# Kernel tuning notes

Hardware: AMD Instinct MI355X
Metric: run time of the kernel (lower is better)

## Reference

```python
import jax, jax.numpy as jnp
import numpy as np

EPS = 1e-12  # torch F.normalize eps

def _l2norm(x):
    n = jnp.linalg.norm(x, axis=-1, keepdims=True)
    return x / jnp.maximum(n, EPS)

def setup_inputs() -> dict:
    key = jax.random.key(0)
    k0, k1, k2, k3 = jax.random.split(key, 4)
    B, S, L, E, N = 16, 2048, 512, 512, 2048
    z = jax.random.normal(k0, (B, S, L), dtype=jnp.float32)
    mask = jnp.ones((B, S), dtype=bool)  # unused by the module's forward body
    # learned params (xavier-ish scales)
    W_in = jax.random.normal(k1, (E, L), dtype=jnp.float32) / np.float32(np.sqrt(L))
    b_in = jnp.zeros((E,), dtype=jnp.float32)
    W_out = jax.random.normal(k2, (L, E), dtype=jnp.float32) / np.float32(np.sqrt(E))
    b_out = jnp.zeros((L,), dtype=jnp.float32)
    emb = jax.random.normal(k3, (N, E), dtype=jnp.float32) / np.float32(np.sqrt(E))
    return {"z": z, "mask": mask, "W_in": W_in, "b_in": b_in, "W_out": W_out, "b_out": b_out, "emb": emb}

def reference(z, mask, W_in, b_in, W_out, b_out, emb):
    B, S, L = z.shape
    zf = z.reshape(B * S, L)
    zf = zf @ W_in.T + b_in                 # (BS, E) input projection
    zf = _l2norm(zf)                        # F.normalize over dim=1
    emb_n = _l2norm(emb)                    # codebook rows normalized in-place in torch
    d = -(zf @ emb_n.T)                     # (BS, N) negative cosine similarity
    min_encoding_indices = jnp.argmin(d, axis=1)   # (BS,)
    zq = emb_n[min_encoding_indices]        # gather codebook vectors (BS, E)
    zq = zq @ W_out.T + b_out               # output projection (BS, L)
    zq = zq.reshape(B, S, L)
    zq = z + jax.lax.stop_gradient(zq - z)  # straight-through estimator
    return zq, min_encoding_indices
```

## Files before the change

### kernel.cpp

```cpp
#include <hip/hip_runtime.h>
#include <math.h>

#define BS_TOK 32768
#define DIM 512
#define NCODE 2048

typedef _Float16 f16x8 __attribute__((ext_vector_type(8)));
typedef _Float16 f16x4 __attribute__((ext_vector_type(4)));
typedef float f32x16 __attribute__((ext_vector_type(16)));

#define LDH 40

#define LGKM0_FENCE asm volatile("s_waitcnt lgkmcnt(0)" ::: "memory")
#define SBAR __builtin_amdgcn_s_barrier()

__global__ __launch_bounds__(256) void k_rownorm_split(
    const float* __restrict__ in, _Float16* __restrict__ hi,
    _Float16* __restrict__ lo, int rstride) {
  const int r = blockIdx.x;
  const int t = threadIdx.x;
  const float* row = in + (size_t)r * DIM;
  float v0 = row[t];
  float v1 = row[t + 256];
  float s = v0 * v0 + v1 * v1;
#pragma unroll
  for (int off = 32; off > 0; off >>= 1) s += __shfl_down(s, off, 64);
  __shared__ float ls[4];
  if ((t & 63) == 0) ls[t >> 6] = s;
  __syncthreads();
  float tot = ls[0] + ls[1] + ls[2] + ls[3];
  float sc = 1.0f / fmaxf(sqrtf(tot), 1e-12f);
  float x0 = v0 * sc, x1 = v1 * sc;
  _Float16 h0 = (_Float16)x0;
  _Float16 h1 = (_Float16)x1;
  _Float16 e0 = (_Float16)((x0 - (float)h0) * 2048.0f);
  _Float16 e1 = (_Float16)((x1 - (float)h1) * 2048.0f);
  _Float16* hrow = hi + (size_t)r * rstride;
  _Float16* lrow = lo + (size_t)r * rstride;
  hrow[t] = h0;
  hrow[t + 256] = h1;
  lrow[t] = e0;
  lrow[t + 256] = e1;
}

__global__ __launch_bounds__(256) void k_split_w(const float* __restrict__ w,
                                                 _Float16* __restrict__ hi,
                                                 _Float16* __restrict__ lo) {
  int t = (blockIdx.x * 256 + threadIdx.x) * 4;
  float4 v = *(const float4*)(w + t);
  f16x4 h, l;
  h.x = (_Float16)v.x; l.x = (_Float16)((v.x - (float)h.x) * 2048.0f);
  h.y = (_Float16)v.y; l.y = (_Float16)((v.y - (float)h.y) * 2048.0f);
  h.z = (_Float16)v.z; l.z = (_Float16)((v.z - (float)h.z) * 2048.0f);
  h.w = (_Float16)v.w; l.w = (_Float16)((v.w - (float)h.w) * 2048.0f);
  *(f16x4*)(hi + t) = h;
  *(f16x4*)(lo + t) = l;
}

__global__ __launch_bounds__(256, 2) void k_gemm_mfma_in(
    const float* __restrict__ A, const _Float16* __restrict__ Bhi,
    const _Float16* __restrict__ Blo, const float* __restrict__ bias,
    _Float16* __restrict__ zf16) {
  __shared__ __align__(16) _Float16 sm[2][4][128 * LDH];
  const int tid = threadIdx.x;
  const int w = tid >> 6, l = tid & 63;
  const int wm = w >> 1, wn = w & 1;
  const int lm = l & 31, lh = l >> 5;
  const int m0 = blockIdx.y * 128;
  const int n0 = blockIdx.x * 128;
  const int arow = tid >> 3;
  const int ac4 = (tid & 7) << 2;
  const int brow = tid >> 2;
  const int bq = (tid & 3) << 3;

  f32x16 aHH[2][2], aX[2][2];
#pragma unroll
  for (int mb = 0; mb < 2; ++mb)
#pragma unroll
    for (int nb = 0; nb < 2; ++nb) {
      aHH[mb][nb] = (f32x16)0.0f;
      aX[mb][nb] = (f32x16)0.0f;
    }

  float4 ar[4];
  f16x8 brh[2], brl[2];

  auto LOADS = [&](int kt) {
#pragma unroll
    for (int i = 0; i < 4; ++i)
      ar[i] =
          *(const float4*)(A + (size_t)(m0 + arow + 32 * i) * DIM + kt * 32 + ac4);
#pragma unroll
    for (int i = 0; i < 2; ++i) {
      const size_t g = (size_t)(n0 + brow + 64 * i) * DIM + kt * 32 + bq;
      brh[i] = *(const f16x8*)(Bhi + g);
      brl[i] = *(const f16x8*)(Blo + g);
    }
  };
  auto WRITES = [&](int b) {
#pragma unroll
    for (int i = 0; i < 4; ++i) {
      f16x4 h, lo4;
      h.x = (_Float16)ar[i].x; lo4.x = (_Float16)((ar[i].x - (float)h.x) * 2048.0f);
      h.y = (_Float16)ar[i].y; lo4.y = (_Float16)((ar[i].y - (float)h.y) * 2048.0f);
      h.z = (_Float16)ar[i].z; lo4.z = (_Float16)((ar[i].z - (float)h.z) * 2048.0f);
      h.w = (_Float16)ar[i].w; lo4.w = (_Float16)((ar[i].w - (float)h.w) * 2048.0f);
      *(f16x4*)(&sm[b][0][(arow + 32 * i) * LDH + ac4]) = h;
      *(f16x4*)(&sm[b][1][(arow + 32 * i) * LDH + ac4]) = lo4;
    }
#pragma unroll
    for (int i = 0; i < 2; ++i) {
      *(f16x8*)(&sm[b][2][(brow + 64 * i) * LDH + bq]) = brh[i];
      *(f16x8*)(&sm[b][3][(brow + 64 * i) * LDH + bq]) = brl[i];
    }
  };

  LOADS(0);
  WRITES(0);
  LOADS(1);
  LGKM0_FENCE;
  SBAR;
  int cur = 0;
  const int NT = DIM / 32;
  for (int t = 0; t < NT; ++t) {
    if (t < NT - 1) WRITES(cur ^ 1);
    if (t < NT - 2) LOADS(t + 2);
#pragma unroll
    for (int c = 0; c < 2; ++c) {
      const int ko = c * 16 + lh * 8;
      f16x8 ah[2], al[2], bh[2], bl[2];
#pragma unroll
      for (int mb = 0; mb < 2; ++mb) {
        int r = wm * 64 + mb * 32 + lm;
        ah[mb] = *(const f16x8*)(&sm[cur][0][r * LDH + ko]);
        al[mb] = *(const f16x8*)(&sm[cur][1][r * LDH + ko]);
      }
#pragma unroll
      for (int nb = 0; nb < 2; ++nb) {
        int r = wn * 64 + nb * 32 + lm;
        bh[nb] = *(const f16x8*)(&sm[cur][2][r * LDH + ko]);
        bl[nb] = *(const f16x8*)(&sm[cur][3][r * LDH + ko]);
      }
#pragma unroll
      for (int mb = 0; mb < 2; ++mb)
#pragma unroll
        for (int nb = 0; nb < 2; ++nb) {
          aHH[mb][nb] = __builtin_amdgcn_mfma_f32_32x32x16_f16(
              ah[mb], bh[nb], aHH[mb][nb], 0, 0, 0);
          aX[mb][nb] = __builtin_amdgcn_mfma_f32_32x32x16_f16(
              ah[mb], bl[nb], aX[mb][nb], 0, 0, 0);
          aX[mb][nb] = __builtin_amdgcn_mfma_f32_32x32x16_f16(
              al[mb], bh[nb], aX[mb][nb], 0, 0, 0);
        }
    }
    LGKM0_FENCE;
    SBAR;
    cur ^= 1;
  }
#pragma unroll
  for (int nb = 0; nb < 2; ++nb) {
    int n = n0 + wn * 64 + nb * 32 + lm;
    float bv = bias[n];
#pragma unroll
    for (int mb = 0; mb < 2; ++mb)
#pragma unroll
      for (int r = 0; r < 16; ++r) {
        int m = m0 + wm * 64 + mb * 32 + (r & 3) + 8 * (r >> 2) + 4 * lh;
        float val = aHH[mb][nb][r] + aX[mb][nb][r] * (1.0f / 2048.0f) + bv;
        _Float16 h = (_Float16)val;
        _Float16 lo = (_Float16)((val - (float)h) * 2048.0f);
        zf16[(size_t)m * 1024 + n] = h;
        zf16[(size_t)m * 1024 + 512 + n] = lo;
      }
  }
}

__global__ __launch_bounds__(256, 2) void k_gemm_codebook(
    const _Float16* __restrict__ Ahi, const _Float16* __restrict__ Alo,
    const _Float16* __restrict__ Bhi, const _Float16* __restrict__ Blo,
    const float* __restrict__ bias, float* __restrict__ table) {
  __shared__ __align__(16) _Float16 sm[2][4][128 * LDH];
  const int tid = threadIdx.x;
  const int w = tid >> 6, l = tid & 63;
  const int wm = w >> 1, wn = w & 1;
  const int lm = l & 31, lh = l >> 5;
  const int m0 = blockIdx.y * 128;
  const int n0 = blockIdx.x * 128;
  const int brow = tid >> 2;
  const int bq = (tid & 3) << 3;

  f32x16 aHH[2][2], aX[2][2];
#pragma unroll
  for (int mb = 0; mb < 2; ++mb)
#pragma unroll
    for (int nb = 0; nb < 2; ++nb) {
      aHH[mb][nb] = (f32x16)0.0f;
      aX[mb][nb] = (f32x16)0.0f;
    }

  f16x8 arh[2], arl[2], brh[2], brl[2];

  auto LOADS = [&](int kt) {
    const int kc = kt * 32 + bq;
#pragma unroll
    for (int i = 0; i < 2; ++i) {
      const size_t ga = (size_t)(m0 + brow + 64 * i) * DIM + kc;
      arh[i] = *(const f16x8*)(Ahi + ga);
      arl[i] = *(const f16x8*)(Alo + ga);
      const size_t g = (size_t)(n0 + brow + 64 * i) * DIM + kc;
      brh[i] = *(const f16x8*)(Bhi + g);
      brl[i] = *(const f16x8*)(Blo + g);
    }
  };
  auto WRITES = [&](int b) {
#pragma unroll
    for (int i = 0; i < 2; ++i) {
      *(f16x8*)(&sm[b][0][(brow + 64 * i) * LDH + bq]) = arh[i];
      *(f16x8*)(&sm[b][1][(brow + 64 * i) * LDH + bq]) = arl[i];
      *(f16x8*)(&sm[b][2][(brow + 64 * i) * LDH + bq]) = brh[i];
      *(f16x8*)(&sm[b][3][(brow + 64 * i) * LDH + bq]) = brl[i];
    }
  };

  LOADS(0);
  WRITES(0);
  LOADS(1);
  LGKM0_FENCE;
  SBAR;
  int cur = 0;
  const int NT = DIM / 32;
  for (int t = 0; t < NT; ++t) {
    if (t < NT - 1) WRITES(cur ^ 1);
    if (t < NT - 2) LOADS(t + 2);
#pragma unroll
    for (int c = 0; c < 2; ++c) {
      const int ko = c * 16 + lh * 8;
      f16x8 ah[2], al[2], bh[2], bl[2];
#pragma unroll
      for (int mb = 0; mb < 2; ++mb) {
        int r = wm * 64 + mb * 32 + lm;
        ah[mb] = *(const f16x8*)(&sm[cur][0][r * LDH + ko]);
        al[mb] = *(const f16x8*)(&sm[cur][1][r * LDH + ko]);
      }
#pragma unroll
      for (int nb = 0; nb < 2; ++nb) {
        int r = wn * 64 + nb * 32 + lm;
        bh[nb] = *(const f16x8*)(&sm[cur][2][r * LDH + ko]);
        bl[nb] = *(const f16x8*)(&sm[cur][3][r * LDH + ko]);
      }
#pragma unroll
      for (int mb = 0; mb < 2; ++mb)
#pragma unroll
        for (int nb = 0; nb < 2; ++nb) {
          aHH[mb][nb] = __builtin_amdgcn_mfma_f32_32x32x16_f16(
              ah[mb], bh[nb], aHH[mb][nb], 0, 0, 0);
          aX[mb][nb] = __builtin_amdgcn_mfma_f32_32x32x16_f16(
              ah[mb], bl[nb], aX[mb][nb], 0, 0, 0);
          aX[mb][nb] = __builtin_amdgcn_mfma_f32_32x32x16_f16(
              al[mb], bh[nb], aX[mb][nb], 0, 0, 0);
        }
    }
    LGKM0_FENCE;
    SBAR;
    cur ^= 1;
  }
#pragma unroll
  for (int nb = 0; nb < 2; ++nb) {
    int n = n0 + wn * 64 + nb * 32 + lm;
    float bv = bias[n];
#pragma unroll
    for (int mb = 0; mb < 2; ++mb)
#pragma unroll
      for (int r = 0; r < 16; ++r) {
        int m = m0 + wm * 64 + mb * 32 + (r & 3) + 8 * (r >> 2) + 4 * lh;
        table[(size_t)m * DIM + n] =
            aHH[mb][nb][r] + aX[mb][nb][r] * (1.0f / 2048.0f) + bv;
      }
  }
}

__global__ __launch_bounds__(256) void k_gather_st(
    const float* __restrict__ z, const float* __restrict__ table,
    const int* __restrict__ idx, float* __restrict__ out) {
  int g = blockIdx.x * 256 + threadIdx.x;
  int m = g >> 7;
  int c = (g & 127) << 2;
  int n = idx[m];
  float4 t = *(const float4*)(table + (size_t)n * DIM + c);
  float4 zv = *(const float4*)(z + (size_t)m * DIM + c);
  float4 o;
  o.x = zv.x + (t.x - zv.x);
  o.y = zv.y + (t.y - zv.y);
  o.z = zv.z + (t.z - zv.z);
  o.w = zv.w + (t.w - zv.w);
  *(float4*)(out + (size_t)m * DIM + c) = o;
}

#define SIMK_BM 128
#define SIMK_BN 128
#define NQUART 4
#define QCODES (NCODE / NQUART)

__global__ __launch_bounds__(256, 4) void k_sim_argmax(
    const _Float16* __restrict__ Apack,
    const _Float16* __restrict__ Bhi, unsigned* __restrict__ cand) {
  __shared__ __align__(16) _Float16 sm[2][2][128 * LDH];
  float* sC = (float*)sm;

  const int tid = threadIdx.x;
  const int w = tid >> 6, l = tid & 63;
  const int wm = w >> 1, wn = w & 1;
  const int lm = l & 31, lh = l >> 5;
  const int q = blockIdx.x & (NQUART - 1);
  const int tokbase = (blockIdx.x >> 2) * SIMK_BM;
  const int code0 = q * QCODES;
  const int brow = tid >> 2;
  const int bq = (tid & 3) << 3;
  const int t_red = tid >> 1, h_red = tid & 1;

  unsigned e0 = 0, e1 = 0, e2 = 0, e3 = 0;

  f16x8 arh[2], brh[2];

  auto LOADS = [&](int nt, int kt) {
    const int kc = kt * 32 + bq;
#pragma unroll
    for (int i = 0; i < 2; ++i) {
      arh[i] =
          *(const f16x8*)(Apack + (size_t)(tokbase + brow + 64 * i) * 1024 + kc);
      brh[i] =
          *(const f16x8*)(Bhi + (size_t)(code0 + nt + brow + 64 * i) * DIM + kc);
    }
  };
  auto WRITES = [&](int b) {
#pragma unroll
    for (int i = 0; i < 2; ++i) {
      *(f16x8*)(&sm[b][0][(brow + 64 * i) * LDH + bq]) = arh[i];
      *(f16x8*)(&sm[b][1][(brow + 64 * i) * LDH + bq]) = brh[i];
    }
  };

  for (int nt = 0; nt < QCODES; nt += SIMK_BN) {
    f32x16 aHH[2][2];
#pragma unroll
    for (int mb = 0; mb < 2; ++mb)
#pragma unroll
      for (int nb = 0; nb < 2; ++nb) aHH[mb][nb] = (f32x16)0.0f;
    __syncthreads();
    LOADS(nt, 0);
    WRITES(0);
    LOADS(nt, 1);
    LGKM0_FENCE;
    SBAR;
    int cur = 0;
    for (int t = 0; t < 16; ++t) {
      if (t < 15) WRITES(cur ^ 1);
      if (t < 14) LOADS(nt, t + 2);
#pragma unroll
      for (int c = 0; c < 2; ++c) {
        const int ko = c * 16 + lh * 8;
        f16x8 ah[2], bh[2];
#pragma unroll
        for (int mb = 0; mb < 2; ++mb)
          ah[mb] = *(const f16x8*)(&sm[cur][0][(wm * 64 + mb * 32 + lm) * LDH + ko]);
#pragma unroll
        for (int nb = 0; nb < 2; ++nb)
          bh[nb] = *(const f16x8*)(&sm[cur][1][(wn * 64 + nb * 32 + lm) * LDH + ko]);
#pragma unroll
        for (int mb = 0; mb < 2; ++mb)
#pragma unroll
          for (int nb = 0; nb < 2; ++nb)
            aHH[mb][nb] = __builtin_amdgcn_mfma_f32_32x32x16_f16(
                ah[mb], bh[nb], aHH[mb][nb], 0, 0, 0);
      }
      LGKM0_FENCE;
      SBAR;
      cur ^= 1;
    }
#pragma unroll
    for (int p = 0; p < 2; ++p) {
      __syncthreads();
      if (wn == p) {
#pragma unroll
        for (int mb = 0; mb < 2; ++mb)
#pragma unroll
          for (int nb = 0; nb < 2; ++nb) {
            int nl = nb * 32 + lm;
#pragma unroll
            for (int r = 0; r < 16; ++r) {
              int m = wm * 64 + mb * 32 + (r & 3) + 8 * (r >> 2) + 4 * lh;
              sC[m * 65 + nl] = aHH[mb][nb][r];
            }
          }
      }
      __syncthreads();
      const float* rowp = &sC[t_red * 65 + h_red * 32];
      const int ncomp = 2047 - (code0 + nt + p * 64 + h_red * 32);
#pragma unroll
      for (int i = 0; i < 32; ++i) {
        float v = rowp[i];
        unsigned s = __float_as_uint(v);
        s = (s & 0x80000000u) ? ~s : (s | 0x80000000u);
        unsigned key = (s & 0xFFFFF800u) | (unsigned)(ncomp - i);
        if (key > e3) {
          unsigned y = key, t2;
          t2 = e0 > y ? e0 : y; y = e0 > y ? y : e0; e0 = t2;
          t2 = e1 > y ? e1 : y; y = e1 > y ? y : e1; e1 = t2;
          t2 = e2 > y ? e2 : y; y = e2 > y ? y : e2; e2 = t2;
          e3 = e3 > y ? e3 : y;
        }
      }
    }
  }
  unsigned o0 = __shfl_xor(e0, 1), o1 = __shfl_xor(e1, 1),
           o2 = __shfl_xor(e2, 1), o3 = __shfl_xor(e3, 1);
#define INS4(x)                                    \
  {                                                \
    unsigned y = (x), t2;                          \
    t2 = e0 > y ? e0 : y; y = e0 > y ? y : e0; e0 = t2; \
    t2 = e1 > y ? e1 : y; y = e1 > y ? y : e1; e1 = t2; \
    t2 = e2 > y ? e2 : y; y = e2 > y ? y : e2; e2 = t2; \
    e3 = e3 > y ? e3 : y;                          \
  }
  INS4(o0) INS4(o1) INS4(o2) INS4(o3)
  if (h_red == 0) {
    unsigned* cp = cand + ((size_t)(tokbase + t_red) * NQUART + q) * 4;
    cp[0] = e0; cp[1] = e1; cp[2] = e2; cp[3] = e3;
  }
}

__global__ __launch_bounds__(256) void k_refine(
    const unsigned* __restrict__ cand, const _Float16* __restrict__ zf16,
    const _Float16* __restrict__ embhi, const _Float16* __restrict__ emblo,
    int* __restrict__ idx, float* __restrict__ idxf) {
  const int tok = (blockIdx.x << 2) + (threadIdx.x >> 6);
  const int lane = threadIdx.x & 63;
  f16x8 zh8 = *(const f16x8*)(zf16 + (size_t)tok * 1024 + lane * 8);
  float ss = 0.0f;
#pragma unroll
  for (int j = 0; j < 8; ++j) {
    float x = (float)zh8[j];
    ss += x * x;
  }
#pragma unroll
  for (int off = 1; off < 64; off <<= 1) ss += __shfl_xor(ss, off);

  unsigned k32 = (lane < 16) ? cand[(size_t)tok * 16 + lane] : 0u;
  unsigned m1 = k32, m2 = 0;
#pragma unroll
  for (int off = 1; off < 64; off <<= 1) {
    unsigned q1 = __shfl_xor(m1, off), q2 = __shfl_xor(m2, off);
    unsigned hi = m1 > q1 ? m1 : q1;
    unsigned lo = m1 > q1 ? q1 : m1;
    unsigned s2 = m2 > q2 ? m2 : q2;
    m2 = lo > s2 ? lo : s2;
    m1 = hi;
  }
  unsigned s1 = m1 & 0xFFFFF800u, s2e = m2 & 0xFFFFF800u;
  float v1 = __uint_as_float((s1 & 0x80000000u) ? (s1 & 0x7FFFFFFFu) : ~s1);
  float v2 = __uint_as_float((s2e & 0x80000000u) ? (s2e & 0x7FFFFFFFu) : ~s2e);
  float theta = 2.0e-3f * sqrtf(ss) +
                9.765625e-4f * (fabsf(v1) + fabsf(v2)) + 1e-6f;
  if (v1 - v2 >= theta) {
    if (lane == 0) {
      int n1 = 2047 - (int)(m1 & 0x7FFu);
      idx[tok] = n1;
      idxf[tok] = (float)n1;
    }
    return;
  }
  const int c = lane & 15, seg = lane >> 4;
  unsigned ck = __shfl(k32, c);
  int n = 2047 - (int)(ck & 0x7FFu);
  const _Float16* zh = zf16 + (size_t)tok * 1024 + seg * 128;
  const _Float16* eh = embhi + (size_t)n * DIM + seg * 128;
  const _Float16* el = emblo + (size_t)n * DIM + seg * 128;
  float s = 0.0f;
#pragma unroll
  for (int d = 0; d < 128; d += 8) {
    f16x8 a = *(const f16x8*)(zh + d);
    f16x8 b = *(const f16x8*)(zh + 512 + d);
    f16x8 e = *(const f16x8*)(eh + d);
    f16x8 f = *(const f16x8*)(el + d);
#pragma unroll
    for (int j = 0; j < 8; ++j)
      s += ((float)a[j] + (float)b[j] * (1.0f / 2048.0f)) *
           ((float)e[j] + (float)f[j] * (1.0f / 2048.0f));
  }
  s += __shfl_xor(s, 16);
  s += __shfl_xor(s, 32);
  unsigned sb = __float_as_uint(s);
  sb = (sb & 0x80000000u) ? ~sb : (sb | 0x80000000u);
  unsigned long long kk =
      ((unsigned long long)sb << 32) | (unsigned)(2047 - n);
  if (lane >= 16) kk = 0ull;
#pragma unroll
  for (int off = 1; off < 16; off <<= 1) {
    unsigned long long o = __shfl_xor(kk, off);
    kk = o > kk ? o : kk;
  }
  if (lane == 0) {
    int nb = 2047 - (int)((unsigned)kk & 0x7FFu);
    idx[tok] = nb;
    idxf[tok] = (float)nb;
  }
}

extern "C" void kernel_launch(void* const* d_in, const int* in_sizes, int n_in,
                              void* d_out, int out_size, void* d_ws,
                              size_t ws_size, hipStream_t stream) {
  const float* z = (const float*)d_in[0];
  const float* W_in = (const float*)d_in[2];
  const float* b_in = (const float*)d_in[3];
  const float* W_out = (const float*)d_in[4];
  const float* b_out = (const float*)d_in[5];
  const float* emb = (const float*)d_in[6];

  float* out = (float*)d_out;
  float* zq = out;
  float* idxf = out + (size_t)BS_TOK * DIM;

  _Float16* embhi = (_Float16*)d_ws;
  _Float16* emblo = embhi + (size_t)NCODE * DIM;
  _Float16* winhi = emblo + (size_t)NCODE * DIM;
  _Float16* winlo = winhi + (size_t)DIM * DIM;
  _Float16* wouthi = winlo + (size_t)DIM * DIM;
  _Float16* woutlo = wouthi + (size_t)DIM * DIM;
  int* idx = (int*)(woutlo + (size_t)DIM * DIM);
  unsigned* cand = (unsigned*)(idx + BS_TOK);
  float* table = (float*)cand;

  _Float16* zf16 = (_Float16*)zq;

  k_split_w<<<DIM * DIM / 1024, 256, 0, stream>>>(W_in, winhi, winlo);
  k_split_w<<<DIM * DIM / 1024, 256, 0, stream>>>(W_out, wouthi, woutlo);
  k_rownorm_split<<<NCODE, 256, 0, stream>>>(emb, embhi, emblo, DIM);
  k_gemm_mfma_in<<<dim3(DIM / 128, BS_TOK / 128), 256, 0, stream>>>(
      z, winhi, winlo, b_in, zf16);
  k_sim_argmax<<<(BS_TOK / SIMK_BM) * NQUART, 256, 0, stream>>>(zf16, embhi,
                                                                cand);
  k_refine<<<BS_TOK / 4, 256, 0, stream>>>(cand, zf16, embhi, emblo, idx,
                                           idxf);
  k_gemm_codebook<<<dim3(DIM / 128, NCODE / 128), 256, 0, stream>>>(
      embhi, emblo, wouthi, woutlo, b_out, table);
  k_gather_st<<<BS_TOK * (DIM / 4) / 256, 256, 0, stream>>>(z, table, idx,
                                                            zq);
}
```

Measured before the change: 392.5 us.

## Load A fragments directly from global into registers, stage only B in LDS

```diff
diff --git a/kernel.cpp b/kernel.cpp
--- a/kernel.cpp
+++ b/kernel.cpp
@@ -301,11 +301,11 @@
 #define NQUART 4
 #define QCODES (NCODE / NQUART)
 
-__global__ __launch_bounds__(256, 4) void k_sim_argmax(
+__global__ __launch_bounds__(256, 3) void k_sim_argmax(
     const _Float16* __restrict__ Apack,
     const _Float16* __restrict__ Bhi, unsigned* __restrict__ cand) {
-  __shared__ __align__(16) _Float16 sm[2][2][128 * LDH];
-  float* sC = (float*)sm;
+  __shared__ __align__(16) _Float16 smem[16640];
+  float* sC = (float*)smem;
 
   const int tid = threadIdx.x;
   const int w = tid >> 6, l = tid & 63;
@@ -320,63 +320,73 @@
 
   unsigned e0 = 0, e1 = 0, e2 = 0, e3 = 0;
 
-  f16x8 arh[2], brh[2];
-
-  auto LOADS = [&](int nt, int kt) {
+  const _Float16* aB0 =
+      Apack + (size_t)(tokbase + wm * 64 + lm) * 1024 + lh * 8;
+  const _Float16* aB1 = aB0 + 32 * 1024;
+
+  f16x8 brh[2];
+  auto LOADB = [&](int nt, int kt) {
     const int kc = kt * 32 + bq;
 #pragma unroll
-    for (int i = 0; i < 2; ++i) {
-      arh[i] =
-          *(const f16x8*)(Apack + (size_t)(tokbase + brow + 64 * i) * 1024 + kc);
+    for (int i = 0; i < 2; ++i)
       brh[i] =
           *(const f16x8*)(Bhi + (size_t)(code0 + nt + brow + 64 * i) * DIM + kc);
-    }
-  };
-  auto WRITES = [&](int b) {
-#pragma unroll
-    for (int i = 0; i < 2; ++i) {
-      *(f16x8*)(&sm[b][0][(brow + 64 * i) * LDH + bq]) = arh[i];
-      *(f16x8*)(&sm[b][1][(brow + 64 * i) * LDH + bq]) = brh[i];
+  };
+  auto WRITEB = [&](int b) {
+#pragma unroll
+    for (int i = 0; i < 2; ++i)
+      *(f16x8*)(&smem[b * 5120 + (brow + 64 * i) * LDH + bq]) = brh[i];
+  };
+  f16x8 aC[2][2], aN[2][2];
+  auto LOADA = [&](int t, f16x8 (&a)[2][2]) {
+#pragma unroll
+    for (int c = 0; c < 2; ++c) {
+      a[c][0] = *(const f16x8*)(aB0 + t * 32 + c * 16);
+      a[c][1] = *(const f16x8*)(aB1 + t * 32 + c * 16);
     }
   };
 
   for (int nt = 0; nt < QCODES; nt += SIMK_BN) {
-    f32x16 aHH[2][2];
+    f32x16 acc[2][2];
 #pragma unroll
     for (int mb = 0; mb < 2; ++mb)
 #pragma unroll
-      for (int nb = 0; nb < 2; ++nb) aHH[mb][nb] = (f32x16)0.0f;
+      for (int nb = 0; nb < 2; ++nb) acc[mb][nb] = (f32x16)0.0f;
     __syncthreads();
-    LOADS(nt, 0);
-    WRITES(0);
-    LOADS(nt, 1);
+    LOADB(nt, 0);
+    WRITEB(0);
+    LOADB(nt, 1);
+    LOADA(0, aC);
     LGKM0_FENCE;
     SBAR;
-    int cur = 0;
-    for (int t = 0; t < 16; ++t) {
-      if (t < 15) WRITES(cur ^ 1);
-      if (t < 14) LOADS(nt, t + 2);
+
+    auto STEP = [&](int t, int cur, f16x8 (&aU)[2][2], f16x8 (&aP)[2][2]) {
+      LOADA(t + 1, aP);
+      if (t < 15) WRITEB(cur ^ 1);
+      if (t < 14) LOADB(nt, t + 2);
 #pragma unroll
       for (int c = 0; c < 2; ++c) {
         const int ko = c * 16 + lh * 8;
-        f16x8 ah[2], bh[2];
+        f16x8 bh[2];
+#pragma unroll
+        for (int nb = 0; nb < 2; ++nb)
+          bh[nb] = *(const f16x8*)(&smem[cur * 5120 +
+                                         (wn * 64 + nb * 32 + lm) * LDH + ko]);
 #pragma unroll
         for (int mb = 0; mb < 2; ++mb)
-          ah[mb] = *(const f16x8*)(&sm[cur][0][(wm * 64 + mb * 32 + lm) * LDH + ko]);
-#pragma unroll
-        for (int nb = 0; nb < 2; ++nb)
-          bh[nb] = *(const f16x8*)(&sm[cur][1][(wn * 64 + nb * 32 + lm) * LDH + ko]);
-#pragma unroll
-        for (int mb = 0; mb < 2; ++mb)
 #pragma unroll
           for (int nb = 0; nb < 2; ++nb)
-            aHH[mb][nb] = __builtin_amdgcn_mfma_f32_32x32x16_f16(
-                ah[mb], bh[nb], aHH[mb][nb], 0, 0, 0);
+            acc[mb][nb] = __builtin_amdgcn_mfma_f32_32x32x16_f16(
+                aU[c][mb], bh[nb], acc[mb][nb], 0, 0, 0);
       }
       LGKM0_FENCE;
       SBAR;
-      cur ^= 1;
-    }
+    };
+    for (int t2 = 0; t2 < 16; t2 += 2) {
+      STEP(t2, 0, aC, aN);
+      STEP(t2 + 1, 1, aN, aC);
+    }
+
 #pragma unroll
     for (int p = 0; p < 2; ++p) {
       __syncthreads();
@@ -389,7 +399,7 @@
 #pragma unroll
             for (int r = 0; r < 16; ++r) {
               int m = wm * 64 + mb * 32 + (r & 3) + 8 * (r >> 2) + 4 * lh;
-              sC[m * 65 + nl] = aHH[mb][nb][r];
+              sC[m * 65 + nl] = acc[mb][nb][r];
             }
           }
       }
```

Measured after the change: 467.1 us. +19.0%, slower.
